# Kernel optimization log

Hardware: AMD Instinct MI355X
Metric: run time of the kernel (lower is better)

Reference implementation:

```python
import jax, jax.numpy as jnp
import numpy as np

EPS = 1e-12  # torch F.normalize default eps
K, C = 64, 128  # num_clusters, dim


def _l2norm(v, axis):
    n = jnp.sqrt(jnp.sum(v * v, axis=axis, keepdims=True))
    return v / jnp.maximum(n, EPS)


def setup_inputs() -> dict:
    key = jax.random.key(0)
    k1, k2, k3, k4 = jax.random.split(key, 4)
    x = jax.random.normal(k1, (32, C, 64, 64), dtype=jnp.float32)
    centroids = jax.random.uniform(k2, (K, C), dtype=jnp.float32)
    # conv weight/bias initialized from centroids like _init_params (alpha=100)
    alpha = 100.0
    conv_w = 2.0 * alpha * centroids                     # [K, C] (1x1 conv)
    conv_b = -alpha * jnp.linalg.norm(centroids, axis=1) # [K]
    return {"x": x, "conv_w": conv_w, "conv_b": conv_b, "centroids": centroids}


def reference(x, conv_w, conv_b, centroids):
    N = x.shape[0]
    # descriptor-wise L2 normalization over channel dim
    x = _l2norm(x, axis=1)
    xf = x.reshape(N, C, -1)  # [N, C, P]
    # 1x1 conv == per-location linear: [N, K, P]
    logits = jnp.einsum('kc,ncp->nkp', conv_w, xf) + conv_b[None, :, None]
    soft_assign = jax.nn.softmax(logits, axis=1)  # softmax over clusters
    # vlad[n,k,c] = sum_p a[n,k,p] * (x[n,c,p] - centroids[k,c])
    # algebraic rewrite avoids the O(N*K*C*P) intermediate (same math)
    vlad = jnp.einsum('nkp,ncp->nkc', soft_assign, xf) \
        - soft_assign.sum(axis=2)[:, :, None] * centroids[None]
    vlad = _l2norm(vlad, axis=2)            # intra-normalization over C
    vlad = vlad.reshape(N, -1)              # [N, K*C]
    vlad = _l2norm(vlad, axis=1)            # global L2 norm
    return vlad
```

## Files before the change

### kernel.cpp

```cpp
#include <hip/hip_runtime.h>

typedef __attribute__((ext_vector_type(2))) float f2;
typedef __attribute__((ext_vector_type(4))) float f4;
typedef __attribute__((ext_vector_type(4))) float f32x4;
typedef __attribute__((ext_vector_type(4))) unsigned u32x4;
typedef __attribute__((ext_vector_type(8))) short bf16x8;

#define NK 64
#define NC 128
#define NP 4096
#define NN 32
#define EPSV 1e-12f

#define PCH 64
#define CPB 4
#define NGRPX (NP / (PCH * CPB))

#define WS_WF_SL 0
#define WS_SS    8192
#define WS_VP    (8192 + 32768)
#define WS_SLAB_TOTAL (WS_VP + NGRPX * NN * NK * NC)

#define FB_VLAD 0
#define FB_S    (NN * NK * NC)
#define FB_G    (FB_S + NN * NK)
#define FB_WF   (FB_G + NN)
#define FB_TOTAL (FB_WF + 8192)

__device__ __forceinline__ unsigned short f2bf(float x) {
  unsigned u = __builtin_bit_cast(unsigned, x);
  u += 0x7fffu + ((u >> 16) & 1u);
  return (unsigned short)(u >> 16);
}
__device__ __forceinline__ float bf2f(unsigned short h) {
  unsigned u = ((unsigned)h) << 16;
  return __builtin_bit_cast(float, u);
}
__device__ __forceinline__ unsigned cvtpk(float a, float b) {
  unsigned r;
  asm volatile("v_cvt_pk_bf16_f32 %0, %1, %2" : "=v"(r) : "v"(a), "v"(b));
  return r;
}
__device__ __forceinline__ float asf(unsigned u) { return __builtin_bit_cast(float, u); }

__device__ __forceinline__ void barrier_lds() {
  asm volatile("s_waitcnt lgkmcnt(0)" ::: "memory");
  __builtin_amdgcn_s_barrier();
  asm volatile("" ::: "memory");
  __builtin_amdgcn_sched_barrier(0);
}

__global__ void nv_zero(float* __restrict__ ws) {
  int i = blockIdx.x * blockDim.x + threadIdx.x;
  int stride = gridDim.x * blockDim.x;
  for (; i < FB_WF; i += stride) ws[i] = 0.0f;
}

__global__ void nv_wfrag(const float* __restrict__ conv_w, unsigned short* __restrict__ wfrag) {
  int idx = blockIdx.x * 256 + threadIdx.x;
  if (idx >= 2048) return;
  int lane = idx & 63, hl = (idx >> 6) & 1, ct = (idx >> 7) & 3, kt = idx >> 9;
  int r = lane & 15, g = lane >> 4;
  const float* src = conv_w + (16 * kt + r) * NC + 32 * ct + 8 * g;
  unsigned short o[8];
#pragma unroll
  for (int j = 0; j < 8; ++j) {
    float v = src[j];
    unsigned short h = f2bf(v);
    o[j] = hl ? f2bf(v - bf2f(h)) : h;
  }
  u32x4 pk;
#pragma unroll
  for (int m = 0; m < 4; ++m) pk[m] = (unsigned)o[2 * m] | ((unsigned)o[2 * m + 1] << 16);
  *reinterpret_cast<u32x4*>(wfrag + (size_t)idx * 8) = pk;
}

template <bool SLAB>
__global__ __launch_bounds__(512, 2)
void nv_main(const float* __restrict__ x, const unsigned short* __restrict__ wfrag,
             const float* __restrict__ conv_b, float* __restrict__ vout,
             float* __restrict__ sout) {
  __shared__ __align__(16) unsigned xhl_t[PCH][132];
  __shared__ __align__(16) unsigned short xh[NC][72];
  __shared__ __align__(16) unsigned short a_lds[NK][72];
  __shared__ __align__(16) float inv_lds[PCH];
  __shared__ __align__(16) float mx_buf[2][PCH];
  __shared__ __align__(16) float sum_buf[2][PCH];

  const int tid = threadIdx.x;
  const int lane = tid & 63;
  const int w = tid >> 6;
  const int r = lane & 15;
  const int g = lane >> 4;
  const int n = blockIdx.y;
  const int p0loc = (w & 3) << 4;
  const int kp = w >> 2;
  const int ktg0 = kp << 1;
  const int kw = w & 3;
  const int ph = w >> 2;

  bf16x8 whi_r[2][4], wlo_r[2][4];
#pragma unroll
  for (int kt2 = 0; kt2 < 2; ++kt2)
#pragma unroll
    for (int ct = 0; ct < 4; ++ct) {
      const size_t slot = (size_t)(((ktg0 + kt2) * 4 + ct) * 2);
      whi_r[kt2][ct] = *reinterpret_cast<const bf16x8*>(wfrag + (slot * 64 + lane) * 8);
      wlo_r[kt2][ct] = *reinterpret_cast<const bf16x8*>(wfrag + ((slot + 1) * 64 + lane) * 8);
    }
  float bb[2];
#pragma unroll
  for (int kt2 = 0; kt2 < 2; ++kt2) bb[kt2] = conv_b[16 * (ktg0 + kt2) + r];

  f32x4 vacc[8];
#pragma unroll
  for (int t = 0; t < 8; ++t) vacc[t] = (f32x4){0.f, 0.f, 0.f, 0.f};
  float s_part[2] = {0.f, 0.f};

  const int cst = tid & 127;
  const int pq = tid >> 7;
  const int swst = ((cst >> 3) & 3) << 3;
  const int pbase = blockIdx.x * (CPB * PCH);
  const float* xrow = x + ((size_t)n * NC + cst) * NP + 16 * pq;

  f4 pre[4];
  unsigned hs[8];

  auto STAGE_XHL = [&]() {
#pragma unroll
    for (int q4 = 0; q4 < 4; ++q4) {
      f4 v = pre[q4];
      const int pl = 16 * pq + 4 * q4;
      unsigned h01 = cvtpk(v[0], v[1]);
      unsigned h23 = cvtpk(v[2], v[3]);
      float r0 = v[0] - asf(h01 << 16);
      float r1 = v[1] - asf(h01 & 0xffff0000u);
      float r2 = v[2] - asf(h23 << 16);
      float r3 = v[3] - asf(h23 & 0xffff0000u);
      unsigned l01 = cvtpk(r0, r1);
      unsigned l23 = cvtpk(r2, r3);
      hs[2 * q4] = h01;
      hs[2 * q4 + 1] = h23;
      xhl_t[pl + 0][cst] = __builtin_amdgcn_perm(h01, l01, 0x05040100u);
      xhl_t[pl + 1][cst] = __builtin_amdgcn_perm(h01, l01, 0x07060302u);
      xhl_t[pl + 2][cst] = __builtin_amdgcn_perm(h23, l23, 0x05040100u);
      xhl_t[pl + 3][cst] = __builtin_amdgcn_perm(h23, l23, 0x07060302u);
    }
  };
  auto WRITE_XH = [&]() {
#pragma unroll
    for (int q4 = 0; q4 < 4; ++q4) {
      const int pp = (16 * pq + 4 * q4) ^ swst;
      *reinterpret_cast<unsigned*>(&xh[cst][pp]) = hs[2 * q4];
      *reinterpret_cast<unsigned*>(&xh[cst][pp + 2]) = hs[2 * q4 + 1];
    }
  };

#pragma unroll
  for (int q4 = 0; q4 < 4; ++q4)
    pre[q4] = *reinterpret_cast<const f4*>(xrow + pbase + 4 * q4);
  STAGE_XHL();
  barrier_lds();

  for (int cc = 0; cc < CPB; ++cc) {
    WRITE_XH();
    if (cc + 1 < CPB) {
      const float* xb = xrow + pbase + (cc + 1) * PCH;
#pragma unroll
      for (int q4 = 0; q4 < 4; ++q4)
        pre[q4] = *reinterpret_cast<const f4*>(xb + 4 * q4);
    }
    f32x4 d1 = {0.f, 0.f, 0.f, 0.f}, d2 = {0.f, 0.f, 0.f, 0.f};
    f32x4 lac[2];
    lac[0] = (f32x4){0.f, 0.f, 0.f, 0.f};
    lac[1] = (f32x4){0.f, 0.f, 0.f, 0.f};
#pragma unroll
    for (int ct = 0; ct < 4; ++ct) {
      const unsigned* row = &xhl_t[p0loc + r][32 * ct + 8 * g];
      u32x4 wA = *reinterpret_cast<const u32x4*>(row);
      u32x4 wB = *reinterpret_cast<const u32x4*>(row + 4);
      unsigned wv8[8] = {wA[0], wA[1], wA[2], wA[3], wB[0], wB[1], wB[2], wB[3]};
      u32x4 hh, ll;
#pragma unroll
      for (int m = 0; m < 4; ++m) {
        hh[m] = __builtin_amdgcn_perm(wv8[2 * m + 1], wv8[2 * m], 0x07060302u);
        ll[m] = __builtin_amdgcn_perm(wv8[2 * m + 1], wv8[2 * m], 0x05040100u);
      }
      bf16x8 Ah = __builtin_bit_cast(bf16x8, hh);
      bf16x8 Al = __builtin_bit_cast(bf16x8, ll);
      d1 = __builtin_amdgcn_mfma_f32_16x16x32_bf16(Ah, Ah, d1, 0, 0, 0);
      d2 = __builtin_amdgcn_mfma_f32_16x16x32_bf16(Ah, Al, d2, 0, 0, 0);
#pragma unroll
      for (int kt2 = 0; kt2 < 2; ++kt2) {
        lac[kt2] = __builtin_amdgcn_mfma_f32_16x16x32_bf16(Ah, whi_r[kt2][ct], lac[kt2], 0, 0, 0);
        lac[kt2] = __builtin_amdgcn_mfma_f32_16x16x32_bf16(Al, whi_r[kt2][ct], lac[kt2], 0, 0, 0);
        lac[kt2] = __builtin_amdgcn_mfma_f32_16x16x32_bf16(Ah, wlo_r[kt2][ct], lac[kt2], 0, 0, 0);
      }
    }
    if ((r >> 2) == g) {
      int i = r & 3;
      float nsq = d1[i] + 2.0f * d2[i];
      inv_lds[p0loc + r] = __builtin_amdgcn_rsqf(fmaxf(nsq, 1e-24f));
    }
    asm volatile("s_waitcnt lgkmcnt(0)" ::: "memory");
    __builtin_amdgcn_sched_barrier(0);
    f4 ivv = *reinterpret_cast<const f4*>(&inv_lds[p0loc + 4 * g]);
    float lt[2][4], e[2][4], mpart[4], sp[4];
#pragma unroll
    for (int kt2 = 0; kt2 < 2; ++kt2)
#pragma unroll
      for (int i = 0; i < 4; ++i) lt[kt2][i] = lac[kt2][i] * ivv[i] + bb[kt2];
#pragma unroll
    for (int i = 0; i < 4; ++i) mpart[i] = fmaxf(lt[0][i], lt[1][i]);
#pragma unroll
    for (int o = 1; o <= 8; o <<= 1)
#pragma unroll
      for (int i = 0; i < 4; ++i) mpart[i] = fmaxf(mpart[i], __shfl_xor(mpart[i], o));
#pragma unroll
    for (int i = 0; i < 4; ++i) sp[i] = 0.f;
#pragma unroll
    for (int kt2 = 0; kt2 < 2; ++kt2)
#pragma unroll
      for (int i = 0; i < 4; ++i) {
        e[kt2][i] = __expf(lt[kt2][i] - mpart[i]);
        sp[i] += e[kt2][i];
      }
#pragma unroll
    for (int o = 1; o <= 8; o <<= 1)
#pragma unroll
      for (int i = 0; i < 4; ++i) sp[i] += __shfl_xor(sp[i], o);
    if (r < 4) mx_buf[kp][p0loc + 4 * g + r] = mpart[r];
    else if (r < 8) sum_buf[kp][p0loc + 4 * g + (r - 4)] = sp[r - 4];
    barrier_lds();
    {
      f4 m0 = *reinterpret_cast<const f4*>(&mx_buf[0][p0loc + 4 * g]);
      f4 m1 = *reinterpret_cast<const f4*>(&mx_buf[1][p0loc + 4 * g]);
      f4 s0 = *reinterpret_cast<const f4*>(&sum_buf[0][p0loc + 4 * g]);
      f4 s1 = *reinterpret_cast<const f4*>(&sum_buf[1][p0loc + 4 * g]);
      float fcorr[4];
#pragma unroll
      for (int i = 0; i < 4; ++i) {
        float m = fmaxf(m0[i], m1[i]);
        float c0 = __expf(m0[i] - m);
        float c1 = __expf(m1[i] - m);
        float tot = s0[i] * c0 + s1[i] * c1;
        fcorr[i] = (kp == 0 ? c0 : c1) * __builtin_amdgcn_rcpf(tot);
      }
#pragma unroll
      for (int kt2 = 0; kt2 < 2; ++kt2) {
        float av[4];
#pragma unroll
        for (int i = 0; i < 4; ++i) {
          float a = e[kt2][i] * fcorr[i];
          s_part[kt2] += a;
          av[i] = a * ivv[i];
        }
        unsigned* arow = reinterpret_cast<unsigned*>(&a_lds[16 * (ktg0 + kt2) + r][p0loc + 4 * g]);
        arow[0] = cvtpk(av[0], av[1]);
        arow[1] = cvtpk(av[2], av[3]);
      }
    }
    barrier_lds();
    {
      bf16x8 af = *reinterpret_cast<const bf16x8*>(&a_lds[16 * kw + r][32 * ph + 8 * g]);
#pragma unroll
      for (int tcl = 0; tcl < 8; ++tcl) {
        const int c = (tcl << 4) + r;
        const int pblk = ((ph << 2) + g) ^ ((c >> 3) & 3);
        bf16x8 bx = *reinterpret_cast<const bf16x8*>(&xh[c][pblk << 3]);
        vacc[tcl] = __builtin_amdgcn_mfma_f32_16x16x32_bf16(af, bx, vacc[tcl], 0, 0, 0);
      }
    }
    if (cc + 1 < CPB) STAGE_XHL();
    barrier_lds();
  }

  float* cbuf = reinterpret_cast<float*>(&xhl_t[0][0]);
  float* s_red = cbuf + 8192;
  if (w < 4) {
#pragma unroll
    for (int tcl = 0; tcl < 8; ++tcl)
#pragma unroll
      for (int i = 0; i < 4; ++i)
        cbuf[kw * 2048 + (4 * g + i) * 128 + (tcl << 4) + r] = vacc[tcl][i];
  }
#pragma unroll
  for (int kt2 = 0; kt2 < 2; ++kt2) {
    float v = s_part[kt2];
    v += __shfl_xor(v, 16);
    v += __shfl_xor(v, 32);
    if (g == 0) s_red[(kp * 4 + (w & 3)) * 32 + kt2 * 16 + r] = v;
  }
  barrier_lds();
  if (w >= 4) {
#pragma unroll
    for (int tcl = 0; tcl < 8; ++tcl)
#pragma unroll
      for (int i = 0; i < 4; ++i) {
        const int idx = kw * 2048 + (4 * g + i) * 128 + (tcl << 4) + r;
        float v = vacc[tcl][i] + cbuf[idx];
        if constexpr (SLAB) cbuf[idx] = v;
        else atomicAdd(&vout[((size_t)n * NK + 16 * kw + 4 * g + i) * NC + (tcl << 4) + r], v);
      }
  }
  if (tid < 64) {
    float S = 0.f;
#pragma unroll
    for (int pt = 0; pt < 4; ++pt) S += s_red[((tid >> 5) * 4 + pt) * 32 + (tid & 31)];
    if constexpr (SLAB) sout[((size_t)blockIdx.x * NN + n) * NK + tid] = S;
    else atomicAdd(&sout[n * NK + tid], S);
  }
  if constexpr (SLAB) {
    barrier_lds();
    float* dst = vout + ((size_t)blockIdx.x * NN + n) * (NK * NC);
#pragma unroll
    for (int m = 0; m < 4; ++m) {
      const int idx = m * 512 + tid;
      *reinterpret_cast<f4*>(dst + 4 * idx) = *reinterpret_cast<const f4*>(cbuf + 4 * idx);
    }
  }
}

__global__ __launch_bounds__(256)
void nv_finalize2(const float* __restrict__ vin, const float* __restrict__ sin,
                  const float* __restrict__ centroids, float* __restrict__ out) {
  const int wv = threadIdx.x >> 6;
  const int lane = threadIdx.x & 63;
  const int k = blockIdx.x * 4 + wv;
  const int n = blockIdx.y;
  const int c0 = lane * 2;
  f2 v = {0.f, 0.f};
#pragma unroll
  for (int sx = 0; sx < NGRPX; ++sx) {
    const float* vr = vin + ((size_t)sx * NN + n) * (NK * NC) + k * NC;
    f2 t = *reinterpret_cast<const f2*>(vr + c0);
    v.x += t.x;
    v.y += t.y;
  }
  float sv = (lane < 16) ? sin[((size_t)lane * NN + n) * NK + k] : 0.f;
#pragma unroll
  for (int o = 1; o <= 8; o <<= 1) sv += __shfl_xor(sv, o);
  float S = __shfl(sv, 0);
  f2 ce = *reinterpret_cast<const f2*>(centroids + k * NC + c0);
  v.x -= S * ce.x;
  v.y -= S * ce.y;
  float ss = v.x * v.x + v.y * v.y;
#pragma unroll
  for (int o = 1; o < 64; o <<= 1) ss += __shfl_xor(ss, o);
  float inv = 0.125f / fmaxf(sqrtf(ss), EPSV);
  f2 ov = {v.x * inv, v.y * inv};
  *reinterpret_cast<f2*>(out + ((size_t)n * NK + k) * NC + c0) = ov;
}

__global__ void nv_finalize(const float* __restrict__ vin, const float* __restrict__ sin,
                            const float* __restrict__ centroids,
                            float* __restrict__ out, float* __restrict__ gnorm) {
  const int k = blockIdx.x;
  const int n = blockIdx.y;
  const int t = threadIdx.x;
  float S = sin[n * NK + k];
  const size_t base = ((size_t)n * NK + k) * NC;
  float v0 = vin[base + t] - S * centroids[k * NC + t];
  float v1 = vin[base + t + 64] - S * centroids[k * NC + t + 64];
  float ss = v0 * v0 + v1 * v1;
#pragma unroll
  for (int off = 1; off < 64; off <<= 1) ss += __shfl_xor(ss, off);
  float inv = 1.0f / fmaxf(sqrtf(ss), EPSV);
  out[base + t] = v0 * inv;
  out[base + t + 64] = v1 * inv;
  if (t == 0) atomicAdd(&gnorm[n], ss * inv * inv);
}

__global__ void nv_scale(float* __restrict__ out, const float* __restrict__ gnorm) {
  int i = blockIdx.x * blockDim.x + threadIdx.x;
  int n = i >> 13;
  out[i] *= 1.0f / fmaxf(sqrtf(gnorm[n]), EPSV);
}

extern "C" void kernel_launch(void* const* d_in, const int* in_sizes, int n_in,
                              void* d_out, int out_size, void* d_ws, size_t ws_size,
                              hipStream_t stream) {
  const float* x = (const float*)d_in[0];
  const float* conv_w = (const float*)d_in[1];
  const float* conv_b = (const float*)d_in[2];
  const float* centroids = (const float*)d_in[3];
  float* out = (float*)d_out;
  float* ws = (float*)d_ws;

  if (ws_size >= (size_t)WS_SLAB_TOTAL * sizeof(float)) {
    unsigned short* wfrag = (unsigned short*)(ws + WS_WF_SL);
    float* sp = ws + WS_SS;
    float* vp = ws + WS_VP;
    nv_wfrag<<<8, 256, 0, stream>>>(conv_w, wfrag);
    nv_main<true><<<dim3(NGRPX, NN), 512, 0, stream>>>(x, wfrag, conv_b, vp, sp);
    nv_finalize2<<<dim3(NK / 4, NN), 256, 0, stream>>>(vp, sp, centroids, out);
  } else {
    float* vlad_acc = ws + FB_VLAD;
    float* s_acc = ws + FB_S;
    float* gnorm = ws + FB_G;
    unsigned short* wfrag = (unsigned short*)(ws + FB_WF);
    nv_zero<<<256, 256, 0, stream>>>(ws);
    nv_wfrag<<<8, 256, 0, stream>>>(conv_w, wfrag);
    nv_main<false><<<dim3(NGRPX, NN), 512, 0, stream>>>(x, wfrag, conv_b, vlad_acc, s_acc);
    nv_finalize<<<dim3(NK, NN), 64, 0, stream>>>(vlad_acc, s_acc, centroids, out, gnorm);
    nv_scale<<<1024, 256, 0, stream>>>(out, gnorm);
  }
}
```

Measured before the change: 44.73 us.

## Drop separate xh LDS buffer, read bf16 hi from swizzled xhl_t, raise occupancy

Removes the separate transposed bf16 xh shared buffer and the WRITE_XH pass. The second MFMA stage now gathers hi halves directly from the interleaved xhl_t array, using scalar LDS reads and perm. xhl_t gains an XOR swizzle on columns to limit bank conflicts. Freeing that LDS and the hs registers lets launch bounds ask for 3 blocks per CU instead of 2. The cost is staging moved into the loop behind an extra barrier, which drops the prior overlap, plus eight scalar LDS loads per tile instead of one vector load.

```diff
diff --git a/kernel.cpp b/kernel.cpp
--- a/kernel.cpp
+++ b/kernel.cpp
@@ -76,12 +76,11 @@
 }
 
 template <bool SLAB>
-__global__ __launch_bounds__(512, 2)
+__global__ __launch_bounds__(512, 3)
 void nv_main(const float* __restrict__ x, const unsigned short* __restrict__ wfrag,
              const float* __restrict__ conv_b, float* __restrict__ vout,
              float* __restrict__ sout) {
   __shared__ __align__(16) unsigned xhl_t[PCH][132];
-  __shared__ __align__(16) unsigned short xh[NC][72];
   __shared__ __align__(16) unsigned short a_lds[NK][72];
   __shared__ __align__(16) float inv_lds[PCH];
   __shared__ __align__(16) float mx_buf[2][PCH];
@@ -119,18 +118,18 @@
 
   const int cst = tid & 127;
   const int pq = tid >> 7;
-  const int swst = ((cst >> 3) & 3) << 3;
   const int pbase = blockIdx.x * (CPB * PCH);
   const float* xrow = x + ((size_t)n * NC + cst) * NP + 16 * pq;
+  const int sxor = (((p0loc + r) >> 3) & 3) << 4;
 
   f4 pre[4];
-  unsigned hs[8];
 
   auto STAGE_XHL = [&]() {
 #pragma unroll
     for (int q4 = 0; q4 < 4; ++q4) {
       f4 v = pre[q4];
       const int pl = 16 * pq + 4 * q4;
+      const int ccs = cst ^ ((((pl >> 3) & 3)) << 4);
       unsigned h01 = cvtpk(v[0], v[1]);
       unsigned h23 = cvtpk(v[2], v[3]);
       float r0 = v[0] - asf(h01 << 16);
@@ -139,31 +138,20 @@
       float r3 = v[3] - asf(h23 & 0xffff0000u);
       unsigned l01 = cvtpk(r0, r1);
       unsigned l23 = cvtpk(r2, r3);
-      hs[2 * q4] = h01;
-      hs[2 * q4 + 1] = h23;
-      xhl_t[pl + 0][cst] = __builtin_amdgcn_perm(h01, l01, 0x05040100u);
-      xhl_t[pl + 1][cst] = __builtin_amdgcn_perm(h01, l01, 0x07060302u);
-      xhl_t[pl + 2][cst] = __builtin_amdgcn_perm(h23, l23, 0x05040100u);
-      xhl_t[pl + 3][cst] = __builtin_amdgcn_perm(h23, l23, 0x07060302u);
-    }
-  };
-  auto WRITE_XH = [&]() {
-#pragma unroll
-    for (int q4 = 0; q4 < 4; ++q4) {
-      const int pp = (16 * pq + 4 * q4) ^ swst;
-      *reinterpret_cast<unsigned*>(&xh[cst][pp]) = hs[2 * q4];
-      *reinterpret_cast<unsigned*>(&xh[cst][pp + 2]) = hs[2 * q4 + 1];
+      xhl_t[pl + 0][ccs] = __builtin_amdgcn_perm(h01, l01, 0x05040100u);
+      xhl_t[pl + 1][ccs] = __builtin_amdgcn_perm(h01, l01, 0x07060302u);
+      xhl_t[pl + 2][ccs] = __builtin_amdgcn_perm(h23, l23, 0x05040100u);
+      xhl_t[pl + 3][ccs] = __builtin_amdgcn_perm(h23, l23, 0x07060302u);
     }
   };
 
 #pragma unroll
   for (int q4 = 0; q4 < 4; ++q4)
     pre[q4] = *reinterpret_cast<const f4*>(xrow + pbase + 4 * q4);
-  STAGE_XHL();
-  barrier_lds();
 
   for (int cc = 0; cc < CPB; ++cc) {
-    WRITE_XH();
+    STAGE_XHL();
+    barrier_lds();
     if (cc + 1 < CPB) {
       const float* xb = xrow + pbase + (cc + 1) * PCH;
 #pragma unroll
@@ -176,7 +164,7 @@
     lac[1] = (f32x4){0.f, 0.f, 0.f, 0.f};
 #pragma unroll
     for (int ct = 0; ct < 4; ++ct) {
-      const unsigned* row = &xhl_t[p0loc + r][32 * ct + 8 * g];
+      const unsigned* row = &xhl_t[p0loc + r][(32 * ct + 8 * g) ^ sxor];
       u32x4 wA = *reinterpret_cast<const u32x4*>(row);
       u32x4 wB = *reinterpret_cast<const u32x4*>(row + 4);
       unsigned wv8[8] = {wA[0], wA[1], wA[2], wA[3], wB[0], wB[1], wB[2], wB[3]};
@@ -263,15 +251,21 @@
     barrier_lds();
     {
       bf16x8 af = *reinterpret_cast<const bf16x8*>(&a_lds[16 * kw + r][32 * ph + 8 * g]);
+      const int prow0 = 8 * (4 * ph + g);
 #pragma unroll
       for (int tcl = 0; tcl < 8; ++tcl) {
-        const int c = (tcl << 4) + r;
-        const int pblk = ((ph << 2) + g) ^ ((c >> 3) & 3);
-        bf16x8 bx = *reinterpret_cast<const bf16x8*>(&xh[c][pblk << 3]);
-        vacc[tcl] = __builtin_amdgcn_mfma_f32_16x16x32_bf16(af, bx, vacc[tcl], 0, 0, 0);
-      }
-    }
-    if (cc + 1 < CPB) STAGE_XHL();
+        const int ccol = ((tcl << 4) + r) ^ (g << 4);
+        unsigned u[8];
+#pragma unroll
+        for (int j = 0; j < 8; ++j) u[j] = xhl_t[prow0 + j][ccol];
+        u32x4 hb;
+#pragma unroll
+        for (int m = 0; m < 4; ++m)
+          hb[m] = __builtin_amdgcn_perm(u[2 * m + 1], u[2 * m], 0x07060302u);
+        vacc[tcl] = __builtin_amdgcn_mfma_f32_16x16x32_bf16(af, __builtin_bit_cast(bf16x8, hb),
+                                                            vacc[tcl], 0, 0, 0);
+      }
+    }
     barrier_lds();
   }
 
```

Result: slower. 68.32 us (+52.7%).
